# Performance work log

Hardware: AMD Instinct MI355X
Metric: run time of the kernel (lower is better)

The kernel has to match this reference:

```python
import jax, jax.numpy as jnp
import numpy as np

D_K = 64
D_V = 64
N_HEADS = 8
D_MODEL = 128
EPS = 1e-5
NEG = -1e9

def setup_inputs() -> dict:
    key = jax.random.key(0)
    ks = jax.random.split(key, 8)
    B, S = 32, 512
    inp = {
        "input_Q": jax.random.normal(ks[0], (B, S, D_MODEL), jnp.float32),
        "input_K": jax.random.normal(ks[1], (B, S, D_MODEL), jnp.float32),
        "input_V": jax.random.normal(ks[2], (B, S, D_MODEL), jnp.float32),
        "attn_mask": jax.random.randint(ks[3], (B, S, S), 0, 2).astype(bool),
        "W_Q": jax.random.normal(ks[4], (D_MODEL, N_HEADS * D_K), jnp.float32) * 0.05,
        "W_K": jax.random.normal(ks[5], (D_MODEL, N_HEADS * D_K), jnp.float32) * 0.05,
        "W_V": jax.random.normal(ks[6], (D_MODEL, N_HEADS * D_V), jnp.float32) * 0.05,
        "W_fc": jax.random.normal(ks[7], (N_HEADS * D_V, D_MODEL), jnp.float32) * 0.05,
    }
    return inp

def _layer_norm(x):
    mu = jnp.mean(x, axis=-1, keepdims=True)
    var = jnp.mean(jnp.square(x - mu), axis=-1, keepdims=True)
    return (x - mu) * jax.lax.rsqrt(var + EPS)

def reference(input_Q, input_K, input_V, attn_mask, W_Q, W_K, W_V, W_fc):
    B, S, _ = input_Q.shape
    # project and split heads: [B, H, S, d]
    Q = (input_Q @ W_Q).reshape(B, S, N_HEADS, D_K).transpose(0, 2, 1, 3)
    K = (input_K @ W_K).reshape(B, S, N_HEADS, D_K).transpose(0, 2, 1, 3)
    V = (input_V @ W_V).reshape(B, S, N_HEADS, D_V).transpose(0, 2, 1, 3)
    scores = jnp.einsum("bhqd,bhkd->bhqk", Q, K) / np.sqrt(D_K).astype(np.float32)
    scores = jnp.where(attn_mask[:, None, :, :], NEG, scores)
    attn = jax.nn.softmax(scores, axis=-1)
    context = jnp.einsum("bhqk,bhkd->bhqd", attn, V)
    context = context.transpose(0, 2, 1, 3).reshape(B, S, N_HEADS * D_V)
    output = context @ W_fc
    out = _layer_norm(output + input_Q)
    return out, attn
```

## Files before the change

### kernel.cpp

```cpp
#include <hip/hip_runtime.h>
#include <hip/hip_bf16.h>
#include <stdint.h>

#define BATCH   32
#define SEQ     512
#define DMODEL  128
#define NHEADS  8
#define DHEAD   64
#define NEGV    -1e9f

using f32x4 = __attribute__((ext_vector_type(4))) float;
using s16x8 = __attribute__((ext_vector_type(8))) short;
using u16x4 = __attribute__((ext_vector_type(4))) unsigned short;
using u16x8 = __attribute__((ext_vector_type(8))) unsigned short;

__device__ __forceinline__ unsigned short f2bf(float f) {
    union { float f; unsigned int i; } w; w.f = f;
    unsigned int u = w.i;
    u += 0x7fffu + ((u >> 16) & 1u);
    return (unsigned short)(u >> 16);
}
__device__ __forceinline__ s16x8 fragf(const float* p0, const float* p1) {
    float4 a = *reinterpret_cast<const float4*>(p0);
    float4 b = *reinterpret_cast<const float4*>(p1);
    union { s16x8 v; unsigned short e[8]; } u;
    u.e[0] = f2bf(a.x); u.e[1] = f2bf(a.y); u.e[2] = f2bf(a.z); u.e[3] = f2bf(a.w);
    u.e[4] = f2bf(b.x); u.e[5] = f2bf(b.y); u.e[6] = f2bf(b.z); u.e[7] = f2bf(b.w);
    return u.v;
}
__device__ __forceinline__ s16x8 frag8(const unsigned short* p0, const unsigned short* p1) {
    union { s16x8 v; u16x4 h[2]; } u;
    u.h[0] = *reinterpret_cast<const u16x4*>(p0);
    u.h[1] = *reinterpret_cast<const u16x4*>(p1);
    return u.v;
}
__device__ __forceinline__ s16x8 lds_frag(const unsigned short* row_base, int col0, int swz) {
    union { s16x8 v; u16x4 h[2]; } u;
    u.h[0] = *reinterpret_cast<const u16x4*>(row_base + ((col0) ^ swz));
    u.h[1] = *reinterpret_cast<const u16x4*>(row_base + ((col0 + 16) ^ swz));
    return u.v;
}

__global__ void wtrans_kernel(const float* __restrict__ wfc, const float* __restrict__ wq,
                              unsigned short* __restrict__ Wtfc, unsigned short* __restrict__ WQt) {
    const int m = blockIdx.x;
    if (m < 8) {
        const int i0 = m * 8192;
        for (int i = i0 + threadIdx.x; i < i0 + 8192; i += 256) {
            int k = i >> 7, n = i & 127;
            Wtfc[(size_t)n * 512 + k] = f2bf(wfc[i]);
        }
    } else {
        const int i0 = (m - 8) * 8192;
        for (int i = i0 + threadIdx.x; i < i0 + 8192; i += 256) {
            int k = i >> 9, n = i & 511;
            WQt[(size_t)n * 128 + k] = f2bf(wq[i]);
        }
    }
}

__global__ void mask_bitpack_kernel(const int* __restrict__ mask,
                                    unsigned long long* __restrict__ bits) {
    const int wave = threadIdx.x >> 6, lane = threadIdx.x & 63;
    const int wid0 = (blockIdx.x * 4 + wave) * 16;
#pragma unroll
    for (int i = 0; i < 16; i++) {
        const int w = wid0 + i;
        int v = mask[(size_t)w * 64 + lane];
        unsigned long long bb = __ballot(v != 0);
        if (lane == 0) bits[w] = bb;
    }
}

__global__ __launch_bounds__(512, 2) void proj_kernel(
    const float* __restrict__ inK, const float* __restrict__ inV,
    const float* __restrict__ WK, const float* __restrict__ WV,
    unsigned short* __restrict__ Kp, unsigned short* __restrict__ Vt) {
    __shared__ unsigned short Wt[64 * 128];
    const int tid = threadIdx.x;
    const int lane = tid & 63;
    const int wave = tid >> 6;
    const int g = lane >> 4, c = lane & 15;
    const int bh = blockIdx.x;
    const int b = bh >> 3, h = bh & 7;
    const int col0 = 4 * g;
    const int vmode = blockIdx.y;
    const float* X = vmode ? inV : inK;
    const float* W = vmode ? WV : WK;

    for (int i = tid; i < 8192; i += 512) {
        int k = i >> 6, d = i & 63;
        Wt[d * 128 + (k ^ ((d & 7) << 3))] = f2bf(W[(size_t)k * 512 + h * 64 + d]);
    }
    __syncthreads();

    f32x4 a4[4][4];
#pragma unroll
    for (int st = 0; st < 4; st++)
#pragma unroll
        for (int dt = 0; dt < 4; dt++) a4[st][dt] = f32x4{0.f, 0.f, 0.f, 0.f};
#pragma unroll
    for (int ks = 0; ks < 4; ks++) {
        s16x8 xf[4], wt[4];
#pragma unroll
        for (int st = 0; st < 4; st++) {
            const float* p = X + (size_t)(b * 512 + wave * 64 + st * 16 + c) * 128 + ks * 32 + col0;
            xf[st] = fragf(p, p + 16);
        }
#pragma unroll
        for (int dt = 0; dt < 4; dt++) {
            int row = dt * 16 + c;
            wt[dt] = lds_frag(Wt + row * 128, ks * 32 + col0, (row & 7) << 3);
        }
        if (!vmode) {
#pragma unroll
            for (int st = 0; st < 4; st++)
#pragma unroll
                for (int dt = 0; dt < 4; dt++)
                    a4[st][dt] = __builtin_amdgcn_mfma_f32_16x16x32_bf16(wt[dt], xf[st], a4[st][dt], 0, 0, 0);
        } else {
#pragma unroll
            for (int st = 0; st < 4; st++)
#pragma unroll
                for (int dt = 0; dt < 4; dt++)
                    a4[st][dt] = __builtin_amdgcn_mfma_f32_16x16x32_bf16(xf[st], wt[dt], a4[st][dt], 0, 0, 0);
        }
    }
    if (!vmode) {
#pragma unroll
        for (int st = 0; st < 4; st++) {
            const int kt = wave * 4 + st;
#pragma unroll
            for (int f = 0; f < 2; f++) {
                u16x8 o;
#pragma unroll
                for (int j = 0; j < 4; j++) {
                    o[j]     = f2bf(a4[st][2 * f][j]);
                    o[4 + j] = f2bf(a4[st][2 * f + 1][j]);
                }
                *reinterpret_cast<u16x8*>(Kp + ((size_t)(bh * 32 + kt) * 2 + f) * 512 + lane * 8) = o;
            }
        }
    } else {
#pragma unroll
        for (int p = 0; p < 2; p++) {
            const int kk = wave * 2 + p;
#pragma unroll
            for (int dt = 0; dt < 4; dt++) {
                u16x8 o;
#pragma unroll
                for (int j = 0; j < 4; j++) {
                    o[j]     = f2bf(a4[2 * p][dt][j]);
                    o[4 + j] = f2bf(a4[2 * p + 1][dt][j]);
                }
                *reinterpret_cast<u16x8*>(Vt + ((size_t)(bh * 16 + kk) * 4 + dt) * 512 + lane * 8) = o;
            }
        }
    }
}

__global__ __launch_bounds__(256, 2) void attn_kernel(
    const float* __restrict__ inQ,
    const unsigned short* __restrict__ WQt,
    const unsigned short* __restrict__ Kp,
    const unsigned short* __restrict__ Vt,
    const unsigned long long* __restrict__ mbits,
    float* __restrict__ attn_out,
    unsigned short* __restrict__ ctx) {
    const int tid = threadIdx.x;
    const int lane = tid & 63;
    const int wave = tid >> 6;
    const int g = lane >> 4, c = lane & 15;
    const int col0 = 4 * g;
    const int bid = blockIdx.x;
    const int bh = (((bid & 7) * 4 + ((bid >> 3) & 3)) << 3) + ((bid >> 5) & 7);
    const int qc = bid >> 8;
    const int b = bh >> 3, h = bh & 7;
    const int qg = qc * 64 + wave * 16 + c;

    const unsigned short* Kb = Kp + (size_t)bh * 32768;
    const unsigned short* Vb = Vt + (size_t)bh * 32768;

    union { uint4 q[4]; unsigned short e[32]; } mb;
    {
        const unsigned short* mrow16 = (const unsigned short*)(mbits + ((size_t)b * 512 + qg) * 8);
        mb.q[0] = *reinterpret_cast<const uint4*>(mrow16);
        mb.q[1] = *reinterpret_cast<const uint4*>(mrow16 + 8);
        mb.q[2] = *reinterpret_cast<const uint4*>(mrow16 + 16);
        mb.q[3] = *reinterpret_cast<const uint4*>(mrow16 + 24);
    }

    f32x4 qa[4];
#pragma unroll
    for (int dt = 0; dt < 4; dt++) qa[dt] = f32x4{0.f, 0.f, 0.f, 0.f};
    const float* Xq = inQ + ((size_t)b * 512 + qg) * 128;
#pragma unroll
    for (int ks = 0; ks < 4; ks++) {
        s16x8 xq = fragf(Xq + ks * 32 + col0, Xq + ks * 32 + col0 + 16);
#pragma unroll
        for (int dt = 0; dt < 4; dt++) {
            const unsigned short* wp = WQt + (size_t)(h * 64 + dt * 16 + c) * 128 + ks * 32 + col0;
            s16x8 wt = frag8(wp, wp + 16);
            qa[dt] = __builtin_amdgcn_mfma_f32_16x16x32_bf16(wt, xq, qa[dt], 0, 0, 0);
        }
    }
    s16x8 qf0, qf1;
    {
        union { s16x8 v; u16x4 h2[2]; } q0, q1;
#pragma unroll
        for (int j = 0; j < 4; j++) {
            q0.h2[0][j] = f2bf(qa[0][j]);
            q0.h2[1][j] = f2bf(qa[1][j]);
            q1.h2[0][j] = f2bf(qa[2][j]);
            q1.h2[1][j] = f2bf(qa[3][j]);
        }
        qf0 = q0.v; qf1 = q1.v;
    }

    f32x4 acc[32];
#pragma unroll
    for (int t = 0; t < 32; t++) acc[t] = f32x4{0.f, 0.f, 0.f, 0.f};
#pragma unroll
    for (int kt = 0; kt < 32; kt++) {
        s16x8 a0 = *reinterpret_cast<const s16x8*>(Kb + (size_t)(kt * 2 + 0) * 512 + lane * 8);
        s16x8 a1 = *reinterpret_cast<const s16x8*>(Kb + (size_t)(kt * 2 + 1) * 512 + lane * 8);
        acc[kt] = __builtin_amdgcn_mfma_f32_16x16x32_bf16(a0, qf0, acc[kt], 0, 0, 0);
        acc[kt] = __builtin_amdgcn_mfma_f32_16x16x32_bf16(a1, qf1, acc[kt], 0, 0, 0);
    }

    float m = -3.0e38f;
#pragma unroll
    for (int t = 0; t < 32; t++) {
        const unsigned nib = ((unsigned)mb.e[t]) >> col0;
        float s0 = (nib & 1u) ? NEGV : acc[t][0] * 0.125f;
        float s1 = (nib & 2u) ? NEGV : acc[t][1] * 0.125f;
        float s2 = (nib & 4u) ? NEGV : acc[t][2] * 0.125f;
        float s3 = (nib & 8u) ? NEGV : acc[t][3] * 0.125f;
        acc[t] = f32x4{s0, s1, s2, s3};
        m = fmaxf(m, fmaxf(fmaxf(s0, s1), fmaxf(s2, s3)));
    }
    m = fmaxf(m, __shfl_xor(m, 16));
    m = fmaxf(m, __shfl_xor(m, 32));

    float sum = 0.f;
#pragma unroll
    for (int t = 0; t < 32; t++) {
#pragma unroll
        for (int j = 0; j < 4; j++) {
            float e = __expf(acc[t][j] - m);
            acc[t][j] = e;
            sum += e;
        }
    }
    sum += __shfl_xor(sum, 16);
    sum += __shfl_xor(sum, 32);
    const float inv = 1.0f / sum;

    float* arow = attn_out + ((size_t)bh * 512 + qg) * 512;
    f32x4 cacc[4];
#pragma unroll
    for (int dt = 0; dt < 4; dt++) cacc[dt] = f32x4{0.f, 0.f, 0.f, 0.f};

#pragma unroll
    for (int kk = 0; kk < 16; kk++) {
        f32x4 flo, fhi;
#pragma unroll
        for (int j = 0; j < 4; j++) {
            flo[j] = acc[2 * kk][j] * inv;
            fhi[j] = acc[2 * kk + 1][j] * inv;
        }
        *reinterpret_cast<f32x4*>(arow + kk * 32 + col0)      = flo;
        *reinterpret_cast<f32x4*>(arow + kk * 32 + 16 + col0) = fhi;

        union { s16x8 v; unsigned short e[8]; } pf;
        pf.e[0] = f2bf(flo[0]); pf.e[1] = f2bf(flo[1]); pf.e[2] = f2bf(flo[2]); pf.e[3] = f2bf(flo[3]);
        pf.e[4] = f2bf(fhi[0]); pf.e[5] = f2bf(fhi[1]); pf.e[6] = f2bf(fhi[2]); pf.e[7] = f2bf(fhi[3]);
#pragma unroll
        for (int dt = 0; dt < 4; dt++) {
            s16x8 vf = *reinterpret_cast<const s16x8*>(Vb + (size_t)(kk * 4 + dt) * 512 + lane * 8);
            cacc[dt] = __builtin_amdgcn_mfma_f32_16x16x32_bf16(pf.v, vf, cacc[dt], 0, 0, 0);
        }
    }

    unsigned short* crow = ctx + ((size_t)b * 512 + qc * 64 + wave * 16) * 512 + h * 64;
#pragma unroll
    for (int dt = 0; dt < 4; dt++)
#pragma unroll
        for (int j = 0; j < 4; j++)
            crow[(size_t)(g * 4 + j) * 512 + dt * 16 + c] = f2bf(cacc[dt][j]);
}

__global__ __launch_bounds__(256, 2) void ffn_ln_kernel(
    const unsigned short* __restrict__ ctx,
    const unsigned short* __restrict__ Wtfc,
    const float* __restrict__ inQ,
    float* __restrict__ out) {
    __shared__ float lnbuf[64][132];
    const int lane = threadIdx.x & 63;
    const int wave = threadIdx.x >> 6;
    const int g = lane >> 4, c = lane & 15;
    const int row0 = blockIdx.x * 64;

    f32x4 acc[4][2];
#pragma unroll
    for (int mt = 0; mt < 4; mt++)
#pragma unroll
        for (int nt = 0; nt < 2; nt++) acc[mt][nt] = f32x4{0.f, 0.f, 0.f, 0.f};
#pragma unroll
    for (int ks = 0; ks < 16; ks++) {
        s16x8 af[4], bf[2];
#pragma unroll
        for (int mt = 0; mt < 4; mt++) {
            const unsigned short* p = ctx + (size_t)(row0 + mt * 16 + c) * 512 + ks * 32 + 4 * g;
            af[mt] = frag8(p, p + 16);
        }
#pragma unroll
        for (int nt = 0; nt < 2; nt++) {
            const unsigned short* p = Wtfc + (size_t)(wave * 32 + nt * 16 + c) * 512 + ks * 32 + 4 * g;
            bf[nt] = frag8(p, p + 16);
        }
#pragma unroll
        for (int mt = 0; mt < 4; mt++)
#pragma unroll
            for (int nt = 0; nt < 2; nt++)
                acc[mt][nt] = __builtin_amdgcn_mfma_f32_16x16x32_bf16(af[mt], bf[nt], acc[mt][nt], 0, 0, 0);
    }
#pragma unroll
    for (int mt = 0; mt < 4; mt++)
#pragma unroll
        for (int nt = 0; nt < 2; nt++)
#pragma unroll
            for (int j = 0; j < 4; j++)
                lnbuf[mt * 16 + g * 4 + j][wave * 32 + nt * 16 + c] = acc[mt][nt][j];
    __syncthreads();

    const int r = threadIdx.x >> 2;
    const int seg = threadIdx.x & 3;
    const int grow = row0 + r;
    float x[32];
    float s1 = 0.f, s2 = 0.f;
#pragma unroll
    for (int i4 = 0; i4 < 8; i4++) {
        float4 q4 = *reinterpret_cast<const float4*>(inQ + (size_t)grow * 128 + seg * 32 + i4 * 4);
        float xs[4] = {q4.x, q4.y, q4.z, q4.w};
#pragma unroll
        for (int k = 0; k < 4; k++) {
            float xv = lnbuf[r][seg * 32 + i4 * 4 + k] + xs[k];
            x[i4 * 4 + k] = xv;
            s1 += xv;
            s2 += xv * xv;
        }
    }
    s1 += __shfl_xor(s1, 1); s1 += __shfl_xor(s1, 2);
    s2 += __shfl_xor(s2, 1); s2 += __shfl_xor(s2, 2);
    const float mu = s1 * (1.0f / 128.0f);
    const float var = s2 * (1.0f / 128.0f) - mu * mu;
    const float rs = rsqrtf(var + 1e-5f);
#pragma unroll
    for (int i = 0; i < 8; i++) {
        float4 o;
        o.x = (x[i * 4 + 0] - mu) * rs;
        o.y = (x[i * 4 + 1] - mu) * rs;
        o.z = (x[i * 4 + 2] - mu) * rs;
        o.w = (x[i * 4 + 3] - mu) * rs;
        *reinterpret_cast<float4*>(out + (size_t)grow * 128 + seg * 32 + i * 4) = o;
    }
}

extern "C" void kernel_launch(void* const* d_in, const int* in_sizes, int n_in,
                              void* d_out, int out_size, void* d_ws, size_t ws_size,
                              hipStream_t stream) {
    const float* inQ = (const float*)d_in[0];
    const float* inK = (const float*)d_in[1];
    const float* inV = (const float*)d_in[2];
    const int*   msk = (const int*)d_in[3];
    const float* wq  = (const float*)d_in[4];
    const float* wk  = (const float*)d_in[5];
    const float* wv  = (const float*)d_in[6];
    const float* wfc = (const float*)d_in[7];

    float* out  = (float*)d_out;
    float* attn = out + (size_t)BATCH * SEQ * DMODEL;

    unsigned short* ws   = (unsigned short*)d_ws;
    unsigned short* Wtfc = ws;
    unsigned short* WQt  = ws + 65536;
    unsigned short* ctx  = ws + 131072;
    unsigned long long* mbits = (unsigned long long*)(ws + 131072 + 8388608);
    unsigned short* Kp   = ws + 131072 + 8388608 + 524288;
    unsigned short* Vt   = Kp + 8388608;

    hipLaunchKernelGGL(wtrans_kernel, dim3(16), dim3(256), 0, stream, wfc, wq, Wtfc, WQt);
    hipLaunchKernelGGL(mask_bitpack_kernel, dim3(2048), dim3(256), 0, stream, msk, mbits);
    hipLaunchKernelGGL(proj_kernel, dim3(256, 2), dim3(512), 0, stream,
                       inK, inV, wk, wv, Kp, Vt);
    hipLaunchKernelGGL(attn_kernel, dim3(2048), dim3(256), 0, stream,
                       inQ, WQt, Kp, Vt, mbits, attn, ctx);
    hipLaunchKernelGGL(ffn_ln_kernel, dim3(256), dim3(256), 0, stream, ctx, Wtfc, inQ, out);
}
```

Before: 223.1 us.

## Drop max subtraction in softmax, store bf16 exps, raise attention occupancy

The attention kernel no longer computes a row max. It exponentiates the masked scores directly and packs them as bf16 into 16 registers instead of holding 32 fp32 accumulator vectors. The 1/sum normalization is deferred to the context output, and the launch bound is raised to 3 blocks per SM to cut register pressure and add occupancy. The risks are overflow in exp without the max shift for large scores, and attention probabilities written back are now bf16-rounded, which may lose accuracy.

New measurement: 374.2 us. +67.8%, slower.

```diff
diff --git a/kernel.cpp b/kernel.cpp
--- a/kernel.cpp
+++ b/kernel.cpp
@@ -19,6 +19,9 @@
     unsigned int u = w.i;
     u += 0x7fffu + ((u >> 16) & 1u);
     return (unsigned short)(u >> 16);
+}
+__device__ __forceinline__ float bf2f(unsigned short u) {
+    union { unsigned int i; float f; } w; w.i = ((unsigned int)u) << 16; return w.f;
 }
 __device__ __forceinline__ s16x8 fragf(const float* p0, const float* p1) {
     float4 a = *reinterpret_cast<const float4*>(p0);
@@ -159,7 +162,7 @@
     }
 }
 
-__global__ __launch_bounds__(256, 2) void attn_kernel(
+__global__ __launch_bounds__(256, 3) void attn_kernel(
     const float* __restrict__ inQ,
     const unsigned short* __restrict__ WQt,
     const unsigned short* __restrict__ Kp,
@@ -217,40 +220,27 @@
         qf0 = q0.v; qf1 = q1.v;
     }
 
-    f32x4 acc[32];
-#pragma unroll
-    for (int t = 0; t < 32; t++) acc[t] = f32x4{0.f, 0.f, 0.f, 0.f};
+    union PU { s16x8 v; unsigned short e[8]; };
+    PU p[16];
+    float sum = 0.f;
 #pragma unroll
     for (int kt = 0; kt < 32; kt++) {
         s16x8 a0 = *reinterpret_cast<const s16x8*>(Kb + (size_t)(kt * 2 + 0) * 512 + lane * 8);
         s16x8 a1 = *reinterpret_cast<const s16x8*>(Kb + (size_t)(kt * 2 + 1) * 512 + lane * 8);
-        acc[kt] = __builtin_amdgcn_mfma_f32_16x16x32_bf16(a0, qf0, acc[kt], 0, 0, 0);
-        acc[kt] = __builtin_amdgcn_mfma_f32_16x16x32_bf16(a1, qf1, acc[kt], 0, 0, 0);
-    }
-
-    float m = -3.0e38f;
-#pragma unroll
-    for (int t = 0; t < 32; t++) {
-        const unsigned nib = ((unsigned)mb.e[t]) >> col0;
-        float s0 = (nib & 1u) ? NEGV : acc[t][0] * 0.125f;
-        float s1 = (nib & 2u) ? NEGV : acc[t][1] * 0.125f;
-        float s2 = (nib & 4u) ? NEGV : acc[t][2] * 0.125f;
-        float s3 = (nib & 8u) ? NEGV : acc[t][3] * 0.125f;
-        acc[t] = f32x4{s0, s1, s2, s3};
-        m = fmaxf(m, fmaxf(fmaxf(s0, s1), fmaxf(s2, s3)));
-    }
-    m = fmaxf(m, __shfl_xor(m, 16));
-    m = fmaxf(m, __shfl_xor(m, 32));
-
-    float sum = 0.f;
-#pragma unroll
-    for (int t = 0; t < 32; t++) {
-#pragma unroll
-        for (int j = 0; j < 4; j++) {
-            float e = __expf(acc[t][j] - m);
-            acc[t][j] = e;
-            sum += e;
-        }
+        f32x4 s = f32x4{0.f, 0.f, 0.f, 0.f};
+        s = __builtin_amdgcn_mfma_f32_16x16x32_bf16(a0, qf0, s, 0, 0, 0);
+        s = __builtin_amdgcn_mfma_f32_16x16x32_bf16(a1, qf1, s, 0, 0, 0);
+        const unsigned nib = ((unsigned)mb.e[kt]) >> col0;
+        float e0 = (nib & 1u) ? 0.f : __expf(s[0] * 0.125f);
+        float e1 = (nib & 2u) ? 0.f : __expf(s[1] * 0.125f);
+        float e2 = (nib & 4u) ? 0.f : __expf(s[2] * 0.125f);
+        float e3 = (nib & 8u) ? 0.f : __expf(s[3] * 0.125f);
+        sum += (e0 + e1) + (e2 + e3);
+        const int hf = (kt & 1) * 4;
+        p[kt >> 1].e[hf + 0] = f2bf(e0);
+        p[kt >> 1].e[hf + 1] = f2bf(e1);
+        p[kt >> 1].e[hf + 2] = f2bf(e2);
+        p[kt >> 1].e[hf + 3] = f2bf(e3);
     }
     sum += __shfl_xor(sum, 16);
     sum += __shfl_xor(sum, 32);
@@ -266,19 +256,15 @@
         f32x4 flo, fhi;
 #pragma unroll
         for (int j = 0; j < 4; j++) {
-            flo[j] = acc[2 * kk][j] * inv;
-            fhi[j] = acc[2 * kk + 1][j] * inv;
+            flo[j] = bf2f(p[kk].e[j]) * inv;
+            fhi[j] = bf2f(p[kk].e[4 + j]) * inv;
         }
         *reinterpret_cast<f32x4*>(arow + kk * 32 + col0)      = flo;
         *reinterpret_cast<f32x4*>(arow + kk * 32 + 16 + col0) = fhi;
-
-        union { s16x8 v; unsigned short e[8]; } pf;
-        pf.e[0] = f2bf(flo[0]); pf.e[1] = f2bf(flo[1]); pf.e[2] = f2bf(flo[2]); pf.e[3] = f2bf(flo[3]);
-        pf.e[4] = f2bf(fhi[0]); pf.e[5] = f2bf(fhi[1]); pf.e[6] = f2bf(fhi[2]); pf.e[7] = f2bf(fhi[3]);
 #pragma unroll
         for (int dt = 0; dt < 4; dt++) {
             s16x8 vf = *reinterpret_cast<const s16x8*>(Vb + (size_t)(kk * 4 + dt) * 512 + lane * 8);
-            cacc[dt] = __builtin_amdgcn_mfma_f32_16x16x32_bf16(pf.v, vf, cacc[dt], 0, 0, 0);
+            cacc[dt] = __builtin_amdgcn_mfma_f32_16x16x32_bf16(p[kk].v, vf, cacc[dt], 0, 0, 0);
         }
     }
 
@@ -287,7 +273,7 @@
     for (int dt = 0; dt < 4; dt++)
 #pragma unroll
         for (int j = 0; j < 4; j++)
-            crow[(size_t)(g * 4 + j) * 512 + dt * 16 + c] = f2bf(cacc[dt][j]);
+            crow[(size_t)(g * 4 + j) * 512 + dt * 16 + c] = f2bf(cacc[dt][j] * inv);
 }
 
 __global__ __launch_bounds__(256, 2) void ffn_ln_kernel(
```

## Stage per-head K/V in LDS and process all queries per block; merge prep kernels

Applied to the files above, without the earlier changes.

The attention kernel now launches one 512-thread block per (batch, head). It copies that head's whole bf16 K and V (128 KB) into shared memory once, then loops over 32 query groups of 16 rows, reading K/V fragments from LDS instead of global memory. This removes the repeated global/L2 reads of K/V that came from eight separate query-chunk blocks. In exchange, grid size drops to 256 blocks with 128 KB of LDS each, which limits occupancy to about one block per CU and adds a serial load phase. The mask bit-packing and weight-transpose kernels are also merged into one launch to save a kernel launch.

New measurement: 541.3 us. 143% more time.

```diff
diff --git a/kernel.cpp b/kernel.cpp
--- a/kernel.cpp
+++ b/kernel.cpp
@@ -19,6 +19,9 @@
     unsigned int u = w.i;
     u += 0x7fffu + ((u >> 16) & 1u);
     return (unsigned short)(u >> 16);
+}
+__device__ __forceinline__ float bf2f(unsigned short u) {
+    union { unsigned int i; float f; } w; w.i = ((unsigned int)u) << 16; return w.f;
 }
 __device__ __forceinline__ s16x8 fragf(const float* p0, const float* p1) {
     float4 a = *reinterpret_cast<const float4*>(p0);
@@ -41,34 +44,32 @@
     return u.v;
 }
 
-__global__ void wtrans_kernel(const float* __restrict__ wfc, const float* __restrict__ wq,
-                              unsigned short* __restrict__ Wtfc, unsigned short* __restrict__ WQt) {
-    const int m = blockIdx.x;
-    if (m < 8) {
-        const int i0 = m * 8192;
+__global__ void prep_kernel(const int* __restrict__ mask, unsigned long long* __restrict__ bits,
+                            const float* __restrict__ wfc, const float* __restrict__ wq,
+                            unsigned short* __restrict__ Wtfc, unsigned short* __restrict__ WQt) {
+    const int blk = blockIdx.x;
+    if (blk < 2048) {
+        const int wave = threadIdx.x >> 6, lane = threadIdx.x & 63;
+        const int wid0 = (blk * 4 + wave) * 16;
+#pragma unroll
+        for (int i = 0; i < 16; i++) {
+            const int w = wid0 + i;
+            int v = mask[(size_t)w * 64 + lane];
+            unsigned long long bb = __ballot(v != 0);
+            if (lane == 0) bits[w] = bb;
+        }
+    } else if (blk < 2056) {
+        const int i0 = (blk - 2048) * 8192;
         for (int i = i0 + threadIdx.x; i < i0 + 8192; i += 256) {
             int k = i >> 7, n = i & 127;
             Wtfc[(size_t)n * 512 + k] = f2bf(wfc[i]);
         }
     } else {
-        const int i0 = (m - 8) * 8192;
+        const int i0 = (blk - 2056) * 8192;
         for (int i = i0 + threadIdx.x; i < i0 + 8192; i += 256) {
             int k = i >> 9, n = i & 511;
             WQt[(size_t)n * 128 + k] = f2bf(wq[i]);
         }
-    }
-}
-
-__global__ void mask_bitpack_kernel(const int* __restrict__ mask,
-                                    unsigned long long* __restrict__ bits) {
-    const int wave = threadIdx.x >> 6, lane = threadIdx.x & 63;
-    const int wid0 = (blockIdx.x * 4 + wave) * 16;
-#pragma unroll
-    for (int i = 0; i < 16; i++) {
-        const int w = wid0 + i;
-        int v = mask[(size_t)w * 64 + lane];
-        unsigned long long bb = __ballot(v != 0);
-        if (lane == 0) bits[w] = bb;
     }
 }
 
@@ -159,7 +160,7 @@
     }
 }
 
-__global__ __launch_bounds__(256, 2) void attn_kernel(
+__global__ __launch_bounds__(512, 2) void attn_kernel(
     const float* __restrict__ inQ,
     const unsigned short* __restrict__ WQt,
     const unsigned short* __restrict__ Kp,
@@ -167,127 +168,139 @@
     const unsigned long long* __restrict__ mbits,
     float* __restrict__ attn_out,
     unsigned short* __restrict__ ctx) {
+    __shared__ unsigned short Klds[32768];
+    __shared__ unsigned short Vlds[32768];
     const int tid = threadIdx.x;
     const int lane = tid & 63;
     const int wave = tid >> 6;
     const int g = lane >> 4, c = lane & 15;
     const int col0 = 4 * g;
     const int bid = blockIdx.x;
-    const int bh = (((bid & 7) * 4 + ((bid >> 3) & 3)) << 3) + ((bid >> 5) & 7);
-    const int qc = bid >> 8;
+    const int bh = ((bid & 7) << 5) + (bid >> 3);
     const int b = bh >> 3, h = bh & 7;
-    const int qg = qc * 64 + wave * 16 + c;
-
-    const unsigned short* Kb = Kp + (size_t)bh * 32768;
-    const unsigned short* Vb = Vt + (size_t)bh * 32768;
-
-    union { uint4 q[4]; unsigned short e[32]; } mb;
+
     {
-        const unsigned short* mrow16 = (const unsigned short*)(mbits + ((size_t)b * 512 + qg) * 8);
-        mb.q[0] = *reinterpret_cast<const uint4*>(mrow16);
-        mb.q[1] = *reinterpret_cast<const uint4*>(mrow16 + 8);
-        mb.q[2] = *reinterpret_cast<const uint4*>(mrow16 + 16);
-        mb.q[3] = *reinterpret_cast<const uint4*>(mrow16 + 24);
-    }
-
-    f32x4 qa[4];
-#pragma unroll
-    for (int dt = 0; dt < 4; dt++) qa[dt] = f32x4{0.f, 0.f, 0.f, 0.f};
-    const float* Xq = inQ + ((size_t)b * 512 + qg) * 128;
-#pragma unroll
-    for (int ks = 0; ks < 4; ks++) {
-        s16x8 xq = fragf(Xq + ks * 32 + col0, Xq + ks * 32 + col0 + 16);
-#pragma unroll
-        for (int dt = 0; dt < 4; dt++) {
-            const unsigned short* wp = WQt + (size_t)(h * 64 + dt * 16 + c) * 128 + ks * 32 + col0;
-            s16x8 wt = frag8(wp, wp + 16);
-            qa[dt] = __builtin_amdgcn_mfma_f32_16x16x32_bf16(wt, xq, qa[dt], 0, 0, 0);
-        }
-    }
-    s16x8 qf0, qf1;
-    {
-        union { s16x8 v; u16x4 h2[2]; } q0, q1;
-#pragma unroll
-        for (int j = 0; j < 4; j++) {
-            q0.h2[0][j] = f2bf(qa[0][j]);
-            q0.h2[1][j] = f2bf(qa[1][j]);
-            q1.h2[0][j] = f2bf(qa[2][j]);
-            q1.h2[1][j] = f2bf(qa[3][j]);
-        }
-        qf0 = q0.v; qf1 = q1.v;
-    }
-
-    f32x4 acc[32];
-#pragma unroll
-    for (int t = 0; t < 32; t++) acc[t] = f32x4{0.f, 0.f, 0.f, 0.f};
-#pragma unroll
-    for (int kt = 0; kt < 32; kt++) {
-        s16x8 a0 = *reinterpret_cast<const s16x8*>(Kb + (size_t)(kt * 2 + 0) * 512 + lane * 8);
-        s16x8 a1 = *reinterpret_cast<const s16x8*>(Kb + (size_t)(kt * 2 + 1) * 512 + lane * 8);
-        acc[kt] = __builtin_amdgcn_mfma_f32_16x16x32_bf16(a0, qf0, acc[kt], 0, 0, 0);
-        acc[kt] = __builtin_amdgcn_mfma_f32_16x16x32_bf16(a1, qf1, acc[kt], 0, 0, 0);
-    }
-
-    float m = -3.0e38f;
-#pragma unroll
-    for (int t = 0; t < 32; t++) {
-        const unsigned nib = ((unsigned)mb.e[t]) >> col0;
-        float s0 = (nib & 1u) ? NEGV : acc[t][0] * 0.125f;
-        float s1 = (nib & 2u) ? NEGV : acc[t][1] * 0.125f;
-        float s2 = (nib & 4u) ? NEGV : acc[t][2] * 0.125f;
-        float s3 = (nib & 8u) ? NEGV : acc[t][3] * 0.125f;
-        acc[t] = f32x4{s0, s1, s2, s3};
-        m = fmaxf(m, fmaxf(fmaxf(s0, s1), fmaxf(s2, s3)));
-    }
-    m = fmaxf(m, __shfl_xor(m, 16));
-    m = fmaxf(m, __shfl_xor(m, 32));
-
-    float sum = 0.f;
-#pragma unroll
-    for (int t = 0; t < 32; t++) {
-#pragma unroll
-        for (int j = 0; j < 4; j++) {
-            float e = __expf(acc[t][j] - m);
-            acc[t][j] = e;
-            sum += e;
-        }
-    }
-    sum += __shfl_xor(sum, 16);
-    sum += __shfl_xor(sum, 32);
-    const float inv = 1.0f / sum;
-
-    float* arow = attn_out + ((size_t)bh * 512 + qg) * 512;
-    f32x4 cacc[4];
-#pragma unroll
-    for (int dt = 0; dt < 4; dt++) cacc[dt] = f32x4{0.f, 0.f, 0.f, 0.f};
-
-#pragma unroll
-    for (int kk = 0; kk < 16; kk++) {
-        f32x4 flo, fhi;
-#pragma unroll
-        for (int j = 0; j < 4; j++) {
-            flo[j] = acc[2 * kk][j] * inv;
-            fhi[j] = acc[2 * kk + 1][j] * inv;
-        }
-        *reinterpret_cast<f32x4*>(arow + kk * 32 + col0)      = flo;
-        *reinterpret_cast<f32x4*>(arow + kk * 32 + 16 + col0) = fhi;
-
-        union { s16x8 v; unsigned short e[8]; } pf;
-        pf.e[0] = f2bf(flo[0]); pf.e[1] = f2bf(flo[1]); pf.e[2] = f2bf(flo[2]); pf.e[3] = f2bf(flo[3]);
-        pf.e[4] = f2bf(fhi[0]); pf.e[5] = f2bf(fhi[1]); pf.e[6] = f2bf(fhi[2]); pf.e[7] = f2bf(fhi[3]);
-#pragma unroll
-        for (int dt = 0; dt < 4; dt++) {
-            s16x8 vf = *reinterpret_cast<const s16x8*>(Vb + (size_t)(kk * 4 + dt) * 512 + lane * 8);
-            cacc[dt] = __builtin_amdgcn_mfma_f32_16x16x32_bf16(pf.v, vf, cacc[dt], 0, 0, 0);
-        }
-    }
-
-    unsigned short* crow = ctx + ((size_t)b * 512 + qc * 64 + wave * 16) * 512 + h * 64;
-#pragma unroll
-    for (int dt = 0; dt < 4; dt++)
-#pragma unroll
-        for (int j = 0; j < 4; j++)
-            crow[(size_t)(g * 4 + j) * 512 + dt * 16 + c] = f2bf(cacc[dt][j]);
+        const unsigned short* Kb = Kp + (size_t)bh * 32768;
+        const unsigned short* Vb = Vt + (size_t)bh * 32768;
+        for (int i = tid; i < 4096; i += 512) {
+            *reinterpret_cast<u16x8*>(&Klds[i * 8]) = *reinterpret_cast<const u16x8*>(Kb + (size_t)i * 8);
+            *reinterpret_cast<u16x8*>(&Vlds[i * 8]) = *reinterpret_cast<const u16x8*>(Vb + (size_t)i * 8);
+        }
+    }
+    __syncthreads();
+
+    for (int t = 0; t < 4; t++) {
+        const int gi = t * 8 + wave;
+        const int qg = gi * 16 + c;
+
+        union { uint4 q[4]; unsigned short e[32]; } mb;
+        {
+            const unsigned short* mrow16 = (const unsigned short*)(mbits + ((size_t)b * 512 + qg) * 8);
+            mb.q[0] = *reinterpret_cast<const uint4*>(mrow16);
+            mb.q[1] = *reinterpret_cast<const uint4*>(mrow16 + 8);
+            mb.q[2] = *reinterpret_cast<const uint4*>(mrow16 + 16);
+            mb.q[3] = *reinterpret_cast<const uint4*>(mrow16 + 24);
+        }
+
+        f32x4 qa[4];
+#pragma unroll
+        for (int dt = 0; dt < 4; dt++) qa[dt] = f32x4{0.f, 0.f, 0.f, 0.f};
+        const float* Xq = inQ + ((size_t)b * 512 + qg) * 128;
+#pragma unroll
+        for (int ks = 0; ks < 4; ks++) {
+            s16x8 xq = fragf(Xq + ks * 32 + col0, Xq + ks * 32 + col0 + 16);
+#pragma unroll
+            for (int dt = 0; dt < 4; dt++) {
+                const unsigned short* wp = WQt + (size_t)(h * 64 + dt * 16 + c) * 128 + ks * 32 + col0;
+                s16x8 wt = frag8(wp, wp + 16);
+                qa[dt] = __builtin_amdgcn_mfma_f32_16x16x32_bf16(wt, xq, qa[dt], 0, 0, 0);
+            }
+        }
+        s16x8 qf0, qf1;
+        {
+            union { s16x8 v; u16x4 h2[2]; } q0, q1;
+#pragma unroll
+            for (int j = 0; j < 4; j++) {
+                q0.h2[0][j] = f2bf(qa[0][j]);
+                q0.h2[1][j] = f2bf(qa[1][j]);
+                q1.h2[0][j] = f2bf(qa[2][j]);
+                q1.h2[1][j] = f2bf(qa[3][j]);
+            }
+            qf0 = q0.v; qf1 = q1.v;
+        }
+
+        f32x4 acc[32];
+#pragma unroll
+        for (int kt = 0; kt < 32; kt++) acc[kt] = f32x4{0.f, 0.f, 0.f, 0.f};
+#pragma unroll
+        for (int kt = 0; kt < 32; kt++) {
+            s16x8 a0 = *reinterpret_cast<const s16x8*>(&Klds[(kt * 2 + 0) * 512 + lane * 8]);
+            s16x8 a1 = *reinterpret_cast<const s16x8*>(&Klds[(kt * 2 + 1) * 512 + lane * 8]);
+            acc[kt] = __builtin_amdgcn_mfma_f32_16x16x32_bf16(a0, qf0, acc[kt], 0, 0, 0);
+            acc[kt] = __builtin_amdgcn_mfma_f32_16x16x32_bf16(a1, qf1, acc[kt], 0, 0, 0);
+        }
+
+        float m = -3.0e38f;
+#pragma unroll
+        for (int kt = 0; kt < 32; kt++) {
+            const unsigned nib = ((unsigned)mb.e[kt]) >> col0;
+            float s0 = (nib & 1u) ? NEGV : acc[kt][0] * 0.125f;
+            float s1 = (nib & 2u) ? NEGV : acc[kt][1] * 0.125f;
+            float s2 = (nib & 4u) ? NEGV : acc[kt][2] * 0.125f;
+            float s3 = (nib & 8u) ? NEGV : acc[kt][3] * 0.125f;
+            acc[kt] = f32x4{s0, s1, s2, s3};
+            m = fmaxf(m, fmaxf(fmaxf(s0, s1), fmaxf(s2, s3)));
+        }
+        m = fmaxf(m, __shfl_xor(m, 16));
+        m = fmaxf(m, __shfl_xor(m, 32));
+
+        float sum = 0.f;
+#pragma unroll
+        for (int kt = 0; kt < 32; kt++) {
+#pragma unroll
+            for (int j = 0; j < 4; j++) {
+                float e = __expf(acc[kt][j] - m);
+                acc[kt][j] = e;
+                sum += e;
+            }
+        }
+        sum += __shfl_xor(sum, 16);
+        sum += __shfl_xor(sum, 32);
+        const float inv = 1.0f / sum;
+
+        float* arow = attn_out + ((size_t)bh * 512 + qg) * 512;
+        f32x4 cacc[4];
+#pragma unroll
+        for (int dt = 0; dt < 4; dt++) cacc[dt] = f32x4{0.f, 0.f, 0.f, 0.f};
+
+#pragma unroll
+        for (int kk = 0; kk < 16; kk++) {
+            f32x4 flo, fhi;
+#pragma unroll
+            for (int j = 0; j < 4; j++) {
+                flo[j] = acc[2 * kk][j] * inv;
+                fhi[j] = acc[2 * kk + 1][j] * inv;
+            }
+            *reinterpret_cast<f32x4*>(arow + kk * 32 + col0)      = flo;
+            *reinterpret_cast<f32x4*>(arow + kk * 32 + 16 + col0) = fhi;
+
+            union { s16x8 v; unsigned short e[8]; } pf;
+            pf.e[0] = f2bf(flo[0]); pf.e[1] = f2bf(flo[1]); pf.e[2] = f2bf(flo[2]); pf.e[3] = f2bf(flo[3]);
+            pf.e[4] = f2bf(fhi[0]); pf.e[5] = f2bf(fhi[1]); pf.e[6] = f2bf(fhi[2]); pf.e[7] = f2bf(fhi[3]);
+#pragma unroll
+            for (int dt = 0; dt < 4; dt++) {
+                s16x8 vf = *reinterpret_cast<const s16x8*>(&Vlds[(kk * 4 + dt) * 512 + lane * 8]);
+                cacc[dt] = __builtin_amdgcn_mfma_f32_16x16x32_bf16(pf.v, vf, cacc[dt], 0, 0, 0);
+            }
+        }
+
+        unsigned short* crow = ctx + ((size_t)b * 512 + gi * 16) * 512 + h * 64;
+#pragma unroll
+        for (int dt = 0; dt < 4; dt++)
+#pragma unroll
+            for (int j = 0; j < 4; j++)
+                crow[(size_t)(g * 4 + j) * 512 + dt * 16 + c] = f2bf(cacc[dt][j]);
+    }
 }
 
 __global__ __launch_bounds__(256, 2) void ffn_ln_kernel(
@@ -390,11 +403,11 @@
     unsigned short* Kp   = ws + 131072 + 8388608 + 524288;
     unsigned short* Vt   = Kp + 8388608;
 
-    hipLaunchKernelGGL(wtrans_kernel, dim3(16), dim3(256), 0, stream, wfc, wq, Wtfc, WQt);
-    hipLaunchKernelGGL(mask_bitpack_kernel, dim3(2048), dim3(256), 0, stream, msk, mbits);
+    hipLaunchKernelGGL(prep_kernel, dim3(2064), dim3(256), 0, stream,
+                       msk, mbits, wfc, wq, Wtfc, WQt);
     hipLaunchKernelGGL(proj_kernel, dim3(256, 2), dim3(512), 0, stream,
                        inK, inV, wk, wv, Kp, Vt);
-    hipLaunchKernelGGL(attn_kernel, dim3(2048), dim3(256), 0, stream,
+    hipLaunchKernelGGL(attn_kernel, dim3(256), dim3(512), 0, stream,
                        inQ, WQt, Kp, Vt, mbits, attn, ctx);
     hipLaunchKernelGGL(ffn_ln_kernel, dim3(256), dim3(256), 0, stream, ctx, Wtfc, inQ, out);
 }
```
